# Performance work log

Measured on AMD Instinct MI355X. Metric: run time of the kernel, lower is better.

The kernel has to match this reference:

```python
import jax, jax.numpy as jnp
import numpy as np

H, D_MODEL, DK, DV = 16, 1024, 64, 64
B, S = 4, 2048
LN_EPS = 1e-6
NEG = -1e9


def setup_inputs() -> dict:
    key = jax.random.key(0)
    ks = jax.random.split(key, 8)
    query = jax.random.normal(ks[0], (B, S, D_MODEL), dtype=jnp.float32)
    k_in = jax.random.normal(ks[1], (B, S, D_MODEL), dtype=jnp.float32)
    v_in = jax.random.normal(ks[2], (B, S, D_MODEL), dtype=jnp.float32)
    mask = jax.random.randint(ks[3], (B, S, S), 0, 2, dtype=jnp.int32)
    sc = 1.0 / np.sqrt(D_MODEL)
    w_qs = jax.random.normal(ks[4], (D_MODEL, H * DK), dtype=jnp.float32) * sc
    w_ks = jax.random.normal(ks[5], (D_MODEL, H * DK), dtype=jnp.float32) * sc
    w_vs = jax.random.normal(ks[6], (D_MODEL, H * DV), dtype=jnp.float32) * sc
    w_out = jax.random.normal(ks[7], (H * DV, D_MODEL), dtype=jnp.float32) * (1.0 / np.sqrt(H * DV))
    ln_g = jnp.ones((D_MODEL,), dtype=jnp.float32)
    ln_b = jnp.zeros((D_MODEL,), dtype=jnp.float32)
    return {"query": query, "key": k_in, "value": v_in, "mask": mask,
            "w_qs": w_qs, "w_ks": w_ks, "w_vs": w_vs, "w_out": w_out,
            "ln_g": ln_g, "ln_b": ln_b}


def reference(query, key, value, mask, w_qs, w_ks, w_vs, w_out, ln_g, ln_b):
    # projections -> [B, H, S, dk/dv]
    q = (query @ w_qs).reshape(B, S, H, DK).transpose(0, 2, 1, 3)
    k = (key @ w_ks).reshape(B, S, H, DK).transpose(0, 2, 1, 3)
    v = (value @ w_vs).reshape(B, S, H, DV).transpose(0, 2, 1, 3)
    scores = jnp.einsum('bhqd,bhkd->bhqk', q, k) / np.sqrt(DK)
    scores = jnp.where(mask[:, None, :, :] == 0, NEG, scores)
    p = jax.nn.softmax(scores, axis=-1)  # dropout = identity in eval
    x = jnp.einsum('bhqk,bhkd->bhqd', p, v)  # [B,H,S,DV]
    x = x.transpose(0, 2, 1, 3).reshape(B, S, H * DV)
    out = x @ w_out + query  # dropout identity, residual
    mu = out.mean(-1, keepdims=True)
    var = out.var(-1, keepdims=True)
    return (out - mu) / jnp.sqrt(var + LN_EPS) * ln_g + ln_b
```

## Files before the change

kernel.cpp:

```cpp
#include <hip/hip_runtime.h>

#define BB   4
#define SS   2048
#define HH   16
#define DM   1024
#define DKV  64
#define LNEPS 1e-6f

#define MD_BF16 0
#define MD_F32  1
#define MD_F16  2

typedef __attribute__((ext_vector_type(8))) short bf16x8;
typedef __attribute__((ext_vector_type(4))) float f32x4;
#define MFMA16(a,b,c) __builtin_amdgcn_mfma_f32_16x16x32_bf16(a,b,c,0,0,0)

__device__ __forceinline__ void gl_lds16(const ushort* g, ushort* l) {
    __builtin_amdgcn_global_load_lds(
        (const __attribute__((address_space(1))) void*)g,
        (__attribute__((address_space(3))) void*)l, 16, 0, 0);
}
__device__ __forceinline__ void wait_vm0_barrier() {
    asm volatile("s_waitcnt vmcnt(0)" ::: "memory");
    __builtin_amdgcn_s_barrier();
}

__device__ __forceinline__ float2 unpack2(unsigned int u) {
    union { unsigned int i; float f; } a, b;
    a.i = u << 16;
    b.i = u & 0xffff0000u;
    return make_float2(a.f, b.f);
}
__device__ __forceinline__ unsigned short f2bf(float f) {
    union { float f; unsigned int i; } c; c.f = f;
    unsigned int u = c.i;
    unsigned int r = u + 0x7fffu + ((u >> 16) & 1u);
    return (unsigned short)(r >> 16);
}
__device__ __forceinline__ unsigned short f2bf_t(float f) {
    union { float f; unsigned int i; } c; c.f = f;
    return (unsigned short)(c.i >> 16);
}
__device__ __forceinline__ float h2f(unsigned int bits16) {
    unsigned short s = (unsigned short)bits16;
    _Float16 x;
    __builtin_memcpy(&x, &s, 2);
    return (float)x;
}
__device__ __forceinline__ void load4m(const void* p, int mode, size_t e0, float* o) {
    if (mode == MD_F32) {
        float4 v = *(const float4*)((const float*)p + e0);
        o[0] = v.x; o[1] = v.y; o[2] = v.z; o[3] = v.w;
    } else {
        uint2 u = *(const uint2*)((const ushort*)p + e0);
        if (mode == MD_BF16) {
            float2 a = unpack2(u.x), b = unpack2(u.y);
            o[0] = a.x; o[1] = a.y; o[2] = b.x; o[3] = b.y;
        } else {
            o[0] = h2f(u.x & 0xFFFFu); o[1] = h2f(u.x >> 16);
            o[2] = h2f(u.y & 0xFFFFu); o[3] = h2f(u.y >> 16);
        }
    }
}
__device__ __forceinline__ float loadS(const void* p, int mode, size_t i) {
    if (mode == MD_F32) return ((const float*)p)[i];
    unsigned short u = ((const ushort*)p)[i];
    if (mode == MD_BF16) { union { unsigned i; float f; } c; c.i = (unsigned)u << 16; return c.f; }
    return h2f(u);
}

__device__ __forceinline__ void loadAraw(const void* p, int m, size_t e, uint4* r) {
    if (m == MD_F32) {
        const float* f = (const float*)p + e;
        r[0] = *(const uint4*)(f);
        r[1] = *(const uint4*)(f + 4);
        r[2] = *(const uint4*)(f + 8);
        r[3] = *(const uint4*)(f + 12);
    } else {
        const ushort* s = (const ushort*)p + e;
        r[0] = *(const uint4*)s;
        r[1] = *(const uint4*)(s + 8);
    }
}
__device__ __forceinline__ void cvtA16(const uint4* r, int m, uint4* o2) {
    union { ushort u[16]; uint4 v[2]; } o;
    if (m == MD_F32) {
        const float* f = (const float*)r;
#pragma unroll
        for (int j = 0; j < 16; ++j) o.u[j] = f2bf(f[j]);
    } else if (m == MD_BF16) {
        o.v[0] = r[0]; o.v[1] = r[1];
    } else {
        const ushort* s = (const ushort*)r;
#pragma unroll
        for (int j = 0; j < 16; ++j) o.u[j] = f2bf(h2f(s[j]));
    }
    o2[0] = o.v[0]; o2[1] = o.v[1];
}

struct SniffArgs { const void* p[10]; int nhalf[10]; };

__global__ void sniff_all(SniffArgs a, int* __restrict__ modes) {
    __shared__ int cE, cO;
    const int slots[9] = {0, 1, 2, 4, 5, 6, 7, 8, 9};
    const int slot = slots[blockIdx.x];
    const ushort* p = (const ushort*)a.p[slot];
    const int nhalf = a.nhalf[slot];
    if (threadIdx.x == 0) { cE = 0; cO = 0; }
    __syncthreads();
    int e = 0, o = 0;
    for (int i = threadIdx.x; i < nhalf; i += 256) {
        unsigned ex = (p[i] >> 7) & 0xFFu;
        int hit = (ex < 100u || ex == 0xFFu) ? 1 : 0;
        if (i & 1) o += hit; else e += hit;
    }
    atomicAdd(&cE, e);
    atomicAdd(&cO, o);
    __syncthreads();
    if (threadIdx.x == 0) {
        int total = cE + cO;
        modes[slot] = (total < 48) ? MD_BF16 : ((cO * 4 < cE) ? MD_F32 : MD_F16);
    }
}

__global__ __launch_bounds__(256) void mpack(
    const int* __restrict__ mask, unsigned int* __restrict__ pm)
{
    const int w = blockIdx.x * 256 + threadIdx.x;
    const int* p = mask + (size_t)w * 32;
    unsigned int bits = 0u;
#pragma unroll
    for (int j = 0; j < 8; ++j) {
        int4 v = *(const int4*)(p + j * 4);
        bits |= (v.x ? 1u : 0u) << (4 * j);
        bits |= (v.y ? 1u : 0u) << (4 * j + 1);
        bits |= (v.z ? 1u : 0u) << (4 * j + 2);
        bits |= (v.w ? 1u : 0u) << (4 * j + 3);
    }
    pm[w] = bits;
}

struct WtArgs { const void* W[3]; ushort* Wt[3]; int slot[3]; };

__device__ __forceinline__ void wtrans_body(
    const void* __restrict__ W, ushort* __restrict__ Wt, int m)
{
    __shared__ ushort T[64][68];
    const int tid = threadIdx.x;
    const int k0 = blockIdx.y * 64, n0 = blockIdx.x * 64;

    const int r = tid >> 2, c = (tid & 3) * 16;
    float t[4];
#pragma unroll
    for (int j = 0; j < 4; ++j) {
        load4m(W, m, (size_t)(k0 + r) * DM + n0 + c + 4 * j, t);
#pragma unroll
        for (int i = 0; i < 4; ++i) T[r][c + 4 * j + i] = f2bf(t[i]);
    }
    __syncthreads();

    const int rn = tid >> 2, ck = (tid & 3) * 16;
    union { ushort u[8]; uint4 v; } p0, p1;
#pragma unroll
    for (int j = 0; j < 8; ++j) { p0.u[j] = T[ck + j][rn]; p1.u[j] = T[ck + 8 + j][rn]; }
    ushort* op = &Wt[(size_t)(n0 + rn) * DM + k0 + ck];
    *(uint4*)op = p0.v;
    *(uint4*)(op + 8) = p1.v;
}

__global__ __launch_bounds__(256) void wtrans3(WtArgs a, const int* __restrict__ modes) {
    const int g = blockIdx.z;
    wtrans_body(a.W[g], a.Wt[g], modes[a.slot[g]]);
}
__global__ __launch_bounds__(256) void wtrans(
    const void* __restrict__ W, ushort* __restrict__ Wt,
    const int* __restrict__ modes, int wslot)
{
    wtrans_body(W, Wt, modes[wslot]);
}

__global__ __launch_bounds__(256, 4) void projqkv(
    const void* __restrict__ Aq, const void* __restrict__ Ak, const void* __restrict__ Av,
    const ushort* __restrict__ Wtq, const ushort* __restrict__ Wtk, const ushort* __restrict__ Wtv,
    ushort* __restrict__ Qo, ushort* __restrict__ Ko, ushort* __restrict__ Vo,
    const int* __restrict__ modes)
{
    __shared__ __align__(16) ushort As[2][128 * 40];
    __shared__ __align__(16) ushort Bs[2][128 * 32];

    const int z = blockIdx.z;
    const void* A = (z == 0) ? Aq : (z == 1) ? Ak : Av;
    const ushort* Wt = (z == 0) ? Wtq : (z == 1) ? Wtk : Wtv;
    ushort* Out = (z == 0) ? Qo : (z == 1) ? Ko : Vo;
    const int vmode = (z == 2);
    const float scale = (z == 0) ? 0.125f : 1.0f;
    const int m = modes[z];

    const int tid = threadIdx.x;
    const int lane = tid & 63, wv = tid >> 6;
    const int quad = lane >> 4, L = lane & 15;
    const int bid = blockIdx.y * gridDim.x + blockIdx.x;
    const int swz = (bid & 7) * 64 + (bid >> 3);
    const int m0 = (swz >> 3) * 128, n0 = (swz & 7) * 128;
    const int wm = (wv >> 1) * 64, wn = (wv & 1) * 64;

    const int e0 = (wv * 2 + 0) * 512 + lane * 8;
    const int e1 = (wv * 2 + 1) * 512 + lane * 8;
    const ushort* gB0 = Wt + (size_t)(n0 + (e0 >> 5)) * DM + (e0 & 31);
    const ushort* gB1 = Wt + (size_t)(n0 + (e1 >> 5)) * DM + (e1 & 31);

    const int arow = tid >> 1, aseg = tid & 1;
    const size_t aoff = (size_t)(m0 + arow) * DM + aseg * 16;
    const int alds = arow * 40 + aseg * 16;

    f32x4 acc[4][4];
#pragma unroll
    for (int i = 0; i < 4; ++i)
#pragma unroll
        for (int j = 0; j < 4; ++j) { acc[i][j][0] = 0.f; acc[i][j][1] = 0.f; acc[i][j][2] = 0.f; acc[i][j][3] = 0.f; }

    {
        gl_lds16(gB0, &Bs[0][e0]);
        gl_lds16(gB1, &Bs[0][e1]);
        uint4 ar[4], ao[2];
        loadAraw(A, m, aoff, ar);
        cvtA16(ar, m, ao);
        *(uint4*)&As[0][alds]     = ao[0];
        *(uint4*)&As[0][alds + 8] = ao[1];
    }
    __syncthreads();

    int cur = 0;
    for (int kt = 0; kt < 31; ++kt) {
        const int kn = (kt + 1) * 32;
        const int nxt = cur ^ 1;
        gl_lds16(gB0 + kn, &Bs[nxt][e0]);
        gl_lds16(gB1 + kn, &Bs[nxt][e1]);
        uint4 ar[4], ao[2];
        loadAraw(A, m, aoff + kn, ar);

        bf16x8 af[4], bfr[4];
#pragma unroll
        for (int tm = 0; tm < 4; ++tm) af[tm] = *(const bf16x8*)&As[cur][(wm + tm * 16 + L) * 40 + quad * 8];
#pragma unroll
        for (int tn = 0; tn < 4; ++tn) bfr[tn] = *(const bf16x8*)&Bs[cur][(wn + tn * 16 + L) * 32 + quad * 8];
#pragma unroll
        for (int tm = 0; tm < 4; ++tm)
#pragma unroll
            for (int tn = 0; tn < 4; ++tn)
                acc[tm][tn] = MFMA16(af[tm], bfr[tn], acc[tm][tn]);

        cvtA16(ar, m, ao);
        *(uint4*)&As[nxt][alds]     = ao[0];
        *(uint4*)&As[nxt][alds + 8] = ao[1];

        __syncthreads();
        cur ^= 1;
    }
    {
        bf16x8 af[4], bfr[4];
#pragma unroll
        for (int tm = 0; tm < 4; ++tm) af[tm] = *(const bf16x8*)&As[cur][(wm + tm * 16 + L) * 40 + quad * 8];
#pragma unroll
        for (int tn = 0; tn < 4; ++tn) bfr[tn] = *(const bf16x8*)&Bs[cur][(wn + tn * 16 + L) * 32 + quad * 8];
#pragma unroll
        for (int tm = 0; tm < 4; ++tm)
#pragma unroll
            for (int tn = 0; tn < 4; ++tn)
                acc[tm][tn] = MFMA16(af[tm], bfr[tn], acc[tm][tn]);
    }

#pragma unroll
    for (int tm = 0; tm < 4; ++tm)
#pragma unroll
        for (int tn = 0; tn < 4; ++tn)
#pragma unroll
            for (int r = 0; r < 4; ++r) {
                const int mm = m0 + wm + tm * 16 + quad * 4 + r;
                const int n = n0 + wn + tn * 16 + L;
                const int b = mm >> 11, s = mm & 2047;
                const int h = n >> 6, d = n & 63;
                const size_t o = vmode
                    ? ((size_t)(b * HH + h) * DKV + d) * SS + s
                    : ((size_t)(b * HH + h) * SS + s) * DKV + d;
                Out[o] = f2bf(acc[tm][tn][r] * scale);
            }
}

__global__ __launch_bounds__(256) void attn_mfma(
    const ushort* __restrict__ Q, const ushort* __restrict__ K,
    const ushort* __restrict__ Vt, const unsigned int* __restrict__ pm,
    ushort* __restrict__ Xo)
{
    __shared__ __align__(16) ushort Ks[64][72];
    __shared__ __align__(16) ushort Vs[64][72];
    __shared__ __align__(16) ushort Ps[64][72];

    const int tid = threadIdx.x;
    const int lane = tid & 63, wv = tid >> 6;
    const int quad = lane >> 4, L = lane & 15;
    const int bid = blockIdx.y * gridDim.x + blockIdx.x;
    const int swz = (bid & 7) * 256 + (bid >> 3);
    const int bh = swz >> 5, b = bh >> 4, h = bh & 15;
    const int q0 = (swz & 31) * 64;

    const ushort* qp = &Q[((size_t)bh * SS + q0 + wv * 16 + L) * DKV + quad * 8];
    const bf16x8 aq0 = *(const bf16x8*)qp;
    const bf16x8 aq1 = *(const bf16x8*)(qp + 32);

    f32x4 O[4];
    float lacc[4];
#pragma unroll
    for (int t = 0; t < 4; ++t) { O[t][0] = 0.f; O[t][1] = 0.f; O[t][2] = 0.f; O[t][3] = 0.f; }
#pragma unroll
    for (int r = 0; r < 4; ++r) lacc[r] = 0.f;

    const int sr = tid >> 2, sg = tid & 3;
    const ushort* kbase = &K[((size_t)bh * SS + sr) * DKV + sg * 16];
    const ushort* vbase = &Vt[((size_t)bh * DKV + sr) * SS + sg * 16];
    const unsigned int* pmr[4];
#pragma unroll
    for (int r = 0; r < 4; ++r)
        pmr[r] = pm + ((size_t)b * SS + q0 + wv * 16 + quad * 4 + r) * 64;

    for (int kt = 0; kt < 32; ++kt) {
        __syncthreads();
        *(uint4*)&Ks[sr][sg * 16]     = *(const uint4*)kbase;
        *(uint4*)&Ks[sr][sg * 16 + 8] = *(const uint4*)(kbase + 8);
        *(uint4*)&Vs[sr][sg * 16]     = *(const uint4*)vbase;
        *(uint4*)&Vs[sr][sg * 16 + 8] = *(const uint4*)(vbase + 8);
        kbase += 64 * DKV;
        vbase += 64;

        uint2 mw[4];
#pragma unroll
        for (int r = 0; r < 4; ++r) mw[r] = *(const uint2*)(pmr[r] + 2 * kt);

        __syncthreads();

        f32x4 sc[4];
        __builtin_amdgcn_s_setprio(1);
#pragma unroll
        for (int t = 0; t < 4; ++t) {
            bf16x8 b0 = *(const bf16x8*)&Ks[t * 16 + L][quad * 8];
            bf16x8 b1 = *(const bf16x8*)&Ks[t * 16 + L][32 + quad * 8];
            f32x4 c; c[0] = 0.f; c[1] = 0.f; c[2] = 0.f; c[3] = 0.f;
            c = MFMA16(aq0, b0, c);
            c = MFMA16(aq1, b1, c);
            sc[t] = c;
        }
        __builtin_amdgcn_s_setprio(0);

#pragma unroll
        for (int r = 0; r < 4; ++r) {
            const unsigned mx = mw[r].x, my = mw[r].y;
#pragma unroll
            for (int t = 0; t < 4; ++t) {
                const float s = fminf(sc[t][r], 30.f);
                const float e = __expf(s);
                const unsigned wsel = (t & 2) ? my : mx;
                const float p = ((wsel >> ((t & 1) * 16 + L)) & 1u) ? e : 0.f;
                lacc[r] += p;
                Ps[wv * 16 + quad * 4 + r][t * 16 + L] = f2bf_t(p);
            }
        }

        bf16x8 ap0 = *(const bf16x8*)&Ps[wv * 16 + L][quad * 8];
        bf16x8 ap1 = *(const bf16x8*)&Ps[wv * 16 + L][32 + quad * 8];
        __builtin_amdgcn_s_setprio(1);
#pragma unroll
        for (int t = 0; t < 4; ++t) {
            bf16x8 v0 = *(const bf16x8*)&Vs[t * 16 + L][quad * 8];
            bf16x8 v1 = *(const bf16x8*)&Vs[t * 16 + L][32 + quad * 8];
            O[t] = MFMA16(ap0, v0, O[t]);
            O[t] = MFMA16(ap1, v1, O[t]);
        }
        __builtin_amdgcn_s_setprio(0);
    }

    float inv[4];
#pragma unroll
    for (int r = 0; r < 4; ++r) {
        float l = lacc[r];
#pragma unroll
        for (int off = 1; off < 16; off <<= 1) l += __shfl_xor(l, off, 64);
        inv[r] = 1.f / l;
    }
#pragma unroll
    for (int t = 0; t < 4; ++t)
#pragma unroll
        for (int r = 0; r < 4; ++r) {
            const int qg = q0 + wv * 16 + quad * 4 + r;
            Xo[((size_t)b * SS + qg) * DM + h * DKV + t * 16 + L] = f2bf(O[t][r] * inv[r]);
        }
}

__global__ __launch_bounds__(256) void oproj_mfma(
    const ushort* __restrict__ Xin, const ushort* __restrict__ Wt,
    const void* __restrict__ Qres, float* __restrict__ Out,
    const int* __restrict__ modes)
{
    __shared__ __align__(16) ushort Asf[2][4096];
    __shared__ __align__(16) ushort Bsf[2][4096];

    const int tid = threadIdx.x;
    const int lane = tid & 63, wv = tid >> 6;
    const int quad = lane >> 4, L = lane & 15;
    const int bid = blockIdx.y * gridDim.x + blockIdx.x;
    const int swz = (bid & 7) * 64 + (bid >> 3);
    const int m0 = (swz >> 3) * 128, n0 = (swz & 7) * 128;
    const int wm = (wv >> 1) * 64, wn = (wv & 1) * 64;
    const int mq = modes[0];

    const int e0 = (wv * 2 + 0) * 512 + lane * 8;
    const int e1 = (wv * 2 + 1) * 512 + lane * 8;
    const ushort* gA0 = Xin + (size_t)(m0 + (e0 >> 5)) * DM + (e0 & 31);
    const ushort* gA1 = Xin + (size_t)(m0 + (e1 >> 5)) * DM + (e1 & 31);
    const ushort* gB0 = Wt  + (size_t)(n0 + (e0 >> 5)) * DM + (e0 & 31);
    const ushort* gB1 = Wt  + (size_t)(n0 + (e1 >> 5)) * DM + (e1 & 31);

    f32x4 acc[4][4];
#pragma unroll
    for (int i = 0; i < 4; ++i)
#pragma unroll
        for (int j = 0; j < 4; ++j) { acc[i][j][0] = 0.f; acc[i][j][1] = 0.f; acc[i][j][2] = 0.f; acc[i][j][3] = 0.f; }

    gl_lds16(gA0, &Asf[0][e0]);
    gl_lds16(gA1, &Asf[0][e1]);
    gl_lds16(gB0, &Bsf[0][e0]);
    gl_lds16(gB1, &Bsf[0][e1]);
    wait_vm0_barrier();

    int cur = 0;
    for (int kt = 0; kt < 31; ++kt) {
        const int kn = (kt + 1) * 32;
        gl_lds16(gA0 + kn, &Asf[cur ^ 1][e0]);
        gl_lds16(gA1 + kn, &Asf[cur ^ 1][e1]);
        gl_lds16(gB0 + kn, &Bsf[cur ^ 1][e0]);
        gl_lds16(gB1 + kn, &Bsf[cur ^ 1][e1]);

        bf16x8 af[4], bfr[4];
#pragma unroll
        for (int tm = 0; tm < 4; ++tm) af[tm] = *(const bf16x8*)&Asf[cur][(wm + tm * 16 + L) * 32 + quad * 8];
#pragma unroll
        for (int tn = 0; tn < 4; ++tn) bfr[tn] = *(const bf16x8*)&Bsf[cur][(wn + tn * 16 + L) * 32 + quad * 8];
#pragma unroll
        for (int tm = 0; tm < 4; ++tm)
#pragma unroll
            for (int tn = 0; tn < 4; ++tn)
                acc[tm][tn] = MFMA16(af[tm], bfr[tn], acc[tm][tn]);

        wait_vm0_barrier();
        cur ^= 1;
    }
    {
        bf16x8 af[4], bfr[4];
#pragma unroll
        for (int tm = 0; tm < 4; ++tm) af[tm] = *(const bf16x8*)&Asf[cur][(wm + tm * 16 + L) * 32 + quad * 8];
#pragma unroll
        for (int tn = 0; tn < 4; ++tn) bfr[tn] = *(const bf16x8*)&Bsf[cur][(wn + tn * 16 + L) * 32 + quad * 8];
#pragma unroll
        for (int tm = 0; tm < 4; ++tm)
#pragma unroll
            for (int tn = 0; tn < 4; ++tn)
                acc[tm][tn] = MFMA16(af[tm], bfr[tn], acc[tm][tn]);
    }

#pragma unroll
    for (int tm = 0; tm < 4; ++tm)
#pragma unroll
        for (int tn = 0; tn < 4; ++tn)
#pragma unroll
            for (int r = 0; r < 4; ++r) {
                const int mm = m0 + wm + tm * 16 + quad * 4 + r;
                const int n = n0 + wn + tn * 16 + L;
                const size_t idx = (size_t)mm * DM + n;
                Out[idx] = acc[tm][tn][r] + loadS(Qres, mq, idx);
            }
}

__global__ __launch_bounds__(256) void ln_k(
    float* __restrict__ Out, const void* __restrict__ G,
    const void* __restrict__ Bt, const int* __restrict__ modes)
{
    const int tid = threadIdx.x, wv = tid >> 6, lane = tid & 63;
    const int row = blockIdx.x * 4 + wv;
    const int mg = modes[8], mb = modes[9];
    const size_t base = (size_t)row * DM + lane * 16;

    float v[16];
    float s = 0.f, q = 0.f;
#pragma unroll
    for (int j = 0; j < 16; j += 4) {
        float4 t = *(const float4*)&Out[base + j];
        v[j] = t.x; v[j+1] = t.y; v[j+2] = t.z; v[j+3] = t.w;
        s += t.x + t.y + t.z + t.w;
        q += t.x*t.x + t.y*t.y + t.z*t.z + t.w*t.w;
    }
#pragma unroll
    for (int off = 1; off < 64; off <<= 1) {
        s += __shfl_xor(s, off, 64);
        q += __shfl_xor(q, off, 64);
    }
    const float mu = s * (1.f / 1024.f);
    const float var = q * (1.f / 1024.f) - mu * mu;
    const float inv = rsqrtf(var + LNEPS);

    float gj[16], bj[16];
#pragma unroll
    for (int j = 0; j < 16; j += 4) {
        load4m(G,  mg, (size_t)lane * 16 + j, gj + j);
        load4m(Bt, mb, (size_t)lane * 16 + j, bj + j);
    }
#pragma unroll
    for (int j = 0; j < 16; j += 4) {
        float4 o;
        o.x = (v[j]   - mu) * inv * gj[j]   + bj[j];
        o.y = (v[j+1] - mu) * inv * gj[j+1] + bj[j+1];
        o.z = (v[j+2] - mu) * inv * gj[j+2] + bj[j+2];
        o.w = (v[j+3] - mu) * inv * gj[j+3] + bj[j+3];
        *(float4*)&Out[base + j] = o;
    }
}

extern "C" void kernel_launch(void* const* d_in, const int* in_sizes, int n_in,
                              void* d_out, int out_size, void* d_ws, size_t ws_size,
                              hipStream_t stream)
{
    const void* query = d_in[0];
    const void* key_i = d_in[1];
    const void* value = d_in[2];
    const int*  mask  = (const int*)d_in[3];
    const void* w_qs  = d_in[4];
    const void* w_ks  = d_in[5];
    const void* w_vs  = d_in[6];
    const void* w_out = d_in[7];
    const void* ln_g  = d_in[8];
    const void* ln_b  = d_in[9];
    float* out = (float*)d_out;

    int* modes = (int*)d_ws;
    const size_t PE = (size_t)BB * HH * SS * DKV;
    ushort* Qw = (ushort*)((char*)d_ws + 256);
    ushort* Kw = Qw + PE;
    ushort* Vw = Kw + PE;
    ushort* Xw = Vw + PE;
    ushort* Wtq  = (ushort*)((char*)d_out + (4  << 20));
    ushort* Wtk  = (ushort*)((char*)d_out + (8  << 20));
    ushort* Wtv  = (ushort*)((char*)d_out + (12 << 20));
    ushort* Wt2  = Qw;
    unsigned int* pmask = (unsigned int*)d_out;

    SniffArgs sa;
    for (int i = 0; i < 10; ++i) {
        sa.p[i] = d_in[i];
        sa.nhalf[i] = in_sizes[i] < 4096 ? in_sizes[i] : 4096;
    }
    sniff_all<<<9, 256, 0, stream>>>(sa, modes);
    mpack<<<2048, 256, 0, stream>>>(mask, pmask);

    WtArgs wa;
    wa.W[0] = w_qs; wa.Wt[0] = Wtq; wa.slot[0] = 4;
    wa.W[1] = w_ks; wa.Wt[1] = Wtk; wa.slot[1] = 5;
    wa.W[2] = w_vs; wa.Wt[2] = Wtv; wa.slot[2] = 6;
    wtrans3<<<dim3(16, 16, 3), 256, 0, stream>>>(wa, modes);

    projqkv<<<dim3(8, 64, 3), 256, 0, stream>>>(
        query, key_i, value, Wtq, Wtk, Wtv, Qw, Kw, Vw, modes);

    attn_mfma<<<dim3(32, 64), 256, 0, stream>>>(Qw, Kw, Vw, pmask, Xw);

    wtrans<<<dim3(16, 16), 256, 0, stream>>>(w_out, Wt2, modes, 7);
    oproj_mfma<<<dim3(8, 64), 256, 0, stream>>>(Xw, Wt2, query, out, modes);
    ln_k<<<2048, 256, 0, stream>>>(out, ln_g, ln_b, modes);
}
```

Baseline: 541.9 us.

## Merge prep kernels, inline dtype sniffing, register-prefetch GEMM pipelines

Folds the mask packing and all four weight transposes into one prep launch and drops the separate sniff kernel. Each kernel now detects input dtypes itself through a per-block sniff, which adds redundant global reads and barriers to every block. The projection and output GEMMs stop using global_load_lds and instead prefetch two k-steps ahead into registers, then store into padded LDS tiles with an explicit lgkmcnt wait and barrier. The output projection writes to a workspace buffer that LayerNorm then reads, so the Wt2 transpose can live in d_out.

```diff
diff --git a/kernel.cpp b/kernel.cpp
--- a/kernel.cpp
+++ b/kernel.cpp
@@ -14,16 +14,6 @@
 typedef __attribute__((ext_vector_type(8))) short bf16x8;
 typedef __attribute__((ext_vector_type(4))) float f32x4;
 #define MFMA16(a,b,c) __builtin_amdgcn_mfma_f32_16x16x32_bf16(a,b,c,0,0,0)
-
-__device__ __forceinline__ void gl_lds16(const ushort* g, ushort* l) {
-    __builtin_amdgcn_global_load_lds(
-        (const __attribute__((address_space(1))) void*)g,
-        (__attribute__((address_space(3))) void*)l, 16, 0, 0);
-}
-__device__ __forceinline__ void wait_vm0_barrier() {
-    asm volatile("s_waitcnt vmcnt(0)" ::: "memory");
-    __builtin_amdgcn_s_barrier();
-}
 
 __device__ __forceinline__ float2 unpack2(unsigned int u) {
     union { unsigned int i; float f; } a, b;
@@ -98,14 +88,9 @@
     o2[0] = o.v[0]; o2[1] = o.v[1];
 }
 
-struct SniffArgs { const void* p[10]; int nhalf[10]; };
-
-__global__ void sniff_all(SniffArgs a, int* __restrict__ modes) {
+__device__ __forceinline__ int sniff_local(const void* p_, int nhalf) {
     __shared__ int cE, cO;
-    const int slots[9] = {0, 1, 2, 4, 5, 6, 7, 8, 9};
-    const int slot = slots[blockIdx.x];
-    const ushort* p = (const ushort*)a.p[slot];
-    const int nhalf = a.nhalf[slot];
+    const ushort* p = (const ushort*)p_;
     if (threadIdx.x == 0) { cE = 0; cO = 0; }
     __syncthreads();
     int e = 0, o = 0;
@@ -117,37 +102,42 @@
     atomicAdd(&cE, e);
     atomicAdd(&cO, o);
     __syncthreads();
-    if (threadIdx.x == 0) {
-        int total = cE + cO;
-        modes[slot] = (total < 48) ? MD_BF16 : ((cO * 4 < cE) ? MD_F32 : MD_F16);
-    }
-}
-
-__global__ __launch_bounds__(256) void mpack(
-    const int* __restrict__ mask, unsigned int* __restrict__ pm)
+    const int total = cE + cO;
+    return (total < 48) ? MD_BF16 : ((cO * 4 < cE) ? MD_F32 : MD_F16);
+}
+
+__global__ __launch_bounds__(256) void prep(
+    const int* __restrict__ mask, unsigned int* __restrict__ pm,
+    const void* __restrict__ w_qs, const void* __restrict__ w_ks,
+    const void* __restrict__ w_vs, const void* __restrict__ w_out,
+    ushort* __restrict__ Wtq, ushort* __restrict__ Wtk,
+    ushort* __restrict__ Wtv, ushort* __restrict__ Wt2)
 {
-    const int w = blockIdx.x * 256 + threadIdx.x;
-    const int* p = mask + (size_t)w * 32;
-    unsigned int bits = 0u;
-#pragma unroll
-    for (int j = 0; j < 8; ++j) {
-        int4 v = *(const int4*)(p + j * 4);
-        bits |= (v.x ? 1u : 0u) << (4 * j);
-        bits |= (v.y ? 1u : 0u) << (4 * j + 1);
-        bits |= (v.z ? 1u : 0u) << (4 * j + 2);
-        bits |= (v.w ? 1u : 0u) << (4 * j + 3);
-    }
-    pm[w] = bits;
-}
-
-struct WtArgs { const void* W[3]; ushort* Wt[3]; int slot[3]; };
-
-__device__ __forceinline__ void wtrans_body(
-    const void* __restrict__ W, ushort* __restrict__ Wt, int m)
-{
+    const int bid = blockIdx.x;
+    if (bid < 2048) {
+        const int w = bid * 256 + threadIdx.x;
+        const int* p = mask + (size_t)w * 32;
+        unsigned int bits = 0u;
+#pragma unroll
+        for (int j = 0; j < 8; ++j) {
+            int4 v = *(const int4*)(p + j * 4);
+            bits |= (v.x ? 1u : 0u) << (4 * j);
+            bits |= (v.y ? 1u : 0u) << (4 * j + 1);
+            bits |= (v.z ? 1u : 0u) << (4 * j + 2);
+            bits |= (v.w ? 1u : 0u) << (4 * j + 3);
+        }
+        pm[w] = bits;
+        return;
+    }
+    const int b2 = bid - 2048;
+    const int g = b2 >> 8, sub = b2 & 255;
+    const void* W = (g == 0) ? w_qs : (g == 1) ? w_ks : (g == 2) ? w_vs : w_out;
+    ushort* Wt = (g == 0) ? Wtq : (g == 1) ? Wtk : (g == 2) ? Wtv : Wt2;
+    const int m = sniff_local(W, 4096);
+
     __shared__ ushort T[64][68];
     const int tid = threadIdx.x;
-    const int k0 = blockIdx.y * 64, n0 = blockIdx.x * 64;
+    const int n0 = (sub & 15) * 64, k0 = (sub >> 4) * 64;
 
     const int r = tid >> 2, c = (tid & 3) * 16;
     float t[4];
@@ -168,25 +158,13 @@
     *(uint4*)(op + 8) = p1.v;
 }
 
-__global__ __launch_bounds__(256) void wtrans3(WtArgs a, const int* __restrict__ modes) {
-    const int g = blockIdx.z;
-    wtrans_body(a.W[g], a.Wt[g], modes[a.slot[g]]);
-}
-__global__ __launch_bounds__(256) void wtrans(
-    const void* __restrict__ W, ushort* __restrict__ Wt,
-    const int* __restrict__ modes, int wslot)
-{
-    wtrans_body(W, Wt, modes[wslot]);
-}
-
-__global__ __launch_bounds__(256, 4) void projqkv(
+__global__ __launch_bounds__(256) void projqkv(
     const void* __restrict__ Aq, const void* __restrict__ Ak, const void* __restrict__ Av,
     const ushort* __restrict__ Wtq, const ushort* __restrict__ Wtk, const ushort* __restrict__ Wtv,
-    ushort* __restrict__ Qo, ushort* __restrict__ Ko, ushort* __restrict__ Vo,
-    const int* __restrict__ modes)
+    ushort* __restrict__ Qo, ushort* __restrict__ Ko, ushort* __restrict__ Vo)
 {
     __shared__ __align__(16) ushort As[2][128 * 40];
-    __shared__ __align__(16) ushort Bs[2][128 * 32];
+    __shared__ __align__(16) ushort Bs[2][128 * 40];
 
     const int z = blockIdx.z;
     const void* A = (z == 0) ? Aq : (z == 1) ? Ak : Av;
@@ -194,7 +172,7 @@
     ushort* Out = (z == 0) ? Qo : (z == 1) ? Ko : Vo;
     const int vmode = (z == 2);
     const float scale = (z == 0) ? 0.125f : 1.0f;
-    const int m = modes[z];
+    const int m = sniff_local(A, 4096);
 
     const int tid = threadIdx.x;
     const int lane = tid & 63, wv = tid >> 6;
@@ -204,14 +182,10 @@
     const int m0 = (swz >> 3) * 128, n0 = (swz & 7) * 128;
     const int wm = (wv >> 1) * 64, wn = (wv & 1) * 64;
 
-    const int e0 = (wv * 2 + 0) * 512 + lane * 8;
-    const int e1 = (wv * 2 + 1) * 512 + lane * 8;
-    const ushort* gB0 = Wt + (size_t)(n0 + (e0 >> 5)) * DM + (e0 & 31);
-    const ushort* gB1 = Wt + (size_t)(n0 + (e1 >> 5)) * DM + (e1 & 31);
-
     const int arow = tid >> 1, aseg = tid & 1;
     const size_t aoff = (size_t)(m0 + arow) * DM + aseg * 16;
-    const int alds = arow * 40 + aseg * 16;
+    const size_t boff = (size_t)(n0 + arow) * DM + aseg * 16;
+    const int slds = arow * 40 + aseg * 16;
 
     f32x4 acc[4][4];
 #pragma unroll
@@ -219,55 +193,56 @@
 #pragma unroll
         for (int j = 0; j < 4; ++j) { acc[i][j][0] = 0.f; acc[i][j][1] = 0.f; acc[i][j][2] = 0.f; acc[i][j][3] = 0.f; }
 
+    uint4 rA0[4], rA1[4], rB0[2], rB1[2];
+
+    loadAraw(A, m, aoff, rA0);
+    rB0[0] = *(const uint4*)(Wt + boff);
+    rB0[1] = *(const uint4*)(Wt + boff + 8);
     {
-        gl_lds16(gB0, &Bs[0][e0]);
-        gl_lds16(gB1, &Bs[0][e1]);
-        uint4 ar[4], ao[2];
-        loadAraw(A, m, aoff, ar);
-        cvtA16(ar, m, ao);
-        *(uint4*)&As[0][alds]     = ao[0];
-        *(uint4*)&As[0][alds + 8] = ao[1];
-    }
-    __syncthreads();
-
-    int cur = 0;
-    for (int kt = 0; kt < 31; ++kt) {
-        const int kn = (kt + 1) * 32;
-        const int nxt = cur ^ 1;
-        gl_lds16(gB0 + kn, &Bs[nxt][e0]);
-        gl_lds16(gB1 + kn, &Bs[nxt][e1]);
-        uint4 ar[4], ao[2];
-        loadAraw(A, m, aoff + kn, ar);
-
-        bf16x8 af[4], bfr[4];
-#pragma unroll
-        for (int tm = 0; tm < 4; ++tm) af[tm] = *(const bf16x8*)&As[cur][(wm + tm * 16 + L) * 40 + quad * 8];
-#pragma unroll
-        for (int tn = 0; tn < 4; ++tn) bfr[tn] = *(const bf16x8*)&Bs[cur][(wn + tn * 16 + L) * 32 + quad * 8];
-#pragma unroll
-        for (int tm = 0; tm < 4; ++tm)
-#pragma unroll
-            for (int tn = 0; tn < 4; ++tn)
-                acc[tm][tn] = MFMA16(af[tm], bfr[tn], acc[tm][tn]);
-
-        cvtA16(ar, m, ao);
-        *(uint4*)&As[nxt][alds]     = ao[0];
-        *(uint4*)&As[nxt][alds + 8] = ao[1];
-
-        __syncthreads();
-        cur ^= 1;
-    }
-    {
-        bf16x8 af[4], bfr[4];
-#pragma unroll
-        for (int tm = 0; tm < 4; ++tm) af[tm] = *(const bf16x8*)&As[cur][(wm + tm * 16 + L) * 40 + quad * 8];
-#pragma unroll
-        for (int tn = 0; tn < 4; ++tn) bfr[tn] = *(const bf16x8*)&Bs[cur][(wn + tn * 16 + L) * 32 + quad * 8];
-#pragma unroll
-        for (int tm = 0; tm < 4; ++tm)
-#pragma unroll
-            for (int tn = 0; tn < 4; ++tn)
-                acc[tm][tn] = MFMA16(af[tm], bfr[tn], acc[tm][tn]);
+        uint4 ao[2]; cvtA16(rA0, m, ao);
+        *(uint4*)&As[0][slds]     = ao[0];
+        *(uint4*)&As[0][slds + 8] = ao[1];
+        *(uint4*)&Bs[0][slds]     = rB0[0];
+        *(uint4*)&Bs[0][slds + 8] = rB0[1];
+    }
+    loadAraw(A, m, aoff + 32, rA1);
+    rB1[0] = *(const uint4*)(Wt + boff + 32);
+    rB1[1] = *(const uint4*)(Wt + boff + 40);
+    asm volatile("s_waitcnt lgkmcnt(0)" ::: "memory");
+    __builtin_amdgcn_s_barrier();
+    __builtin_amdgcn_sched_barrier(0);
+
+#define G_MFMA(P)                                                              \
+    { bf16x8 af[4], bfr[4];                                                    \
+      _Pragma("unroll") for (int tm = 0; tm < 4; ++tm)                         \
+          af[tm] = *(const bf16x8*)&As[P][(wm + tm * 16 + L) * 40 + quad * 8]; \
+      _Pragma("unroll") for (int tn = 0; tn < 4; ++tn)                         \
+          bfr[tn] = *(const bf16x8*)&Bs[P][(wn + tn * 16 + L) * 40 + quad * 8];\
+      _Pragma("unroll") for (int tm = 0; tm < 4; ++tm)                         \
+      _Pragma("unroll") for (int tn = 0; tn < 4; ++tn)                         \
+          acc[tm][tn] = MFMA16(af[tm], bfr[tn], acc[tm][tn]); }
+
+#define QKV_ITER(T, P, RAc, RBc, RAn, RBn)                                     \
+    { if ((T) + 2 < 32) {                                                      \
+          loadAraw(A, m, aoff + ((T) + 2) * 32, RAn);                          \
+          RBn[0] = *(const uint4*)(Wt + boff + ((T) + 2) * 32);                \
+          RBn[1] = *(const uint4*)(Wt + boff + ((T) + 2) * 32 + 8);            \
+      }                                                                        \
+      G_MFMA(P)                                                                \
+      if ((T) + 1 < 32) {                                                      \
+          uint4 ao[2]; cvtA16(RAc, m, ao);                                     \
+          *(uint4*)&As[(P) ^ 1][slds]     = ao[0];                             \
+          *(uint4*)&As[(P) ^ 1][slds + 8] = ao[1];                             \
+          *(uint4*)&Bs[(P) ^ 1][slds]     = RBc[0];                            \
+          *(uint4*)&Bs[(P) ^ 1][slds + 8] = RBc[1];                            \
+          asm volatile("s_waitcnt lgkmcnt(0)" ::: "memory");                   \
+          __builtin_amdgcn_s_barrier();                                        \
+          __builtin_amdgcn_sched_barrier(0);                                   \
+      } }
+
+    for (int tt = 0; tt < 16; ++tt) {
+        QKV_ITER(2 * tt,     0, rA1, rB1, rA0, rB0)
+        QKV_ITER(2 * tt + 1, 1, rA0, rB0, rA1, rB1)
     }
 
 #pragma unroll
@@ -397,11 +372,12 @@
 
 __global__ __launch_bounds__(256) void oproj_mfma(
     const ushort* __restrict__ Xin, const ushort* __restrict__ Wt,
-    const void* __restrict__ Qres, float* __restrict__ Out,
-    const int* __restrict__ modes)
+    const void* __restrict__ Qres, float* __restrict__ OutF)
 {
-    __shared__ __align__(16) ushort Asf[2][4096];
-    __shared__ __align__(16) ushort Bsf[2][4096];
+    __shared__ __align__(16) ushort As[2][128 * 40];
+    __shared__ __align__(16) ushort Bs[2][128 * 40];
+
+    const int mq = sniff_local(Qres, 4096);
 
     const int tid = threadIdx.x;
     const int lane = tid & 63, wv = tid >> 6;
@@ -410,14 +386,11 @@
     const int swz = (bid & 7) * 64 + (bid >> 3);
     const int m0 = (swz >> 3) * 128, n0 = (swz & 7) * 128;
     const int wm = (wv >> 1) * 64, wn = (wv & 1) * 64;
-    const int mq = modes[0];
-
-    const int e0 = (wv * 2 + 0) * 512 + lane * 8;
-    const int e1 = (wv * 2 + 1) * 512 + lane * 8;
-    const ushort* gA0 = Xin + (size_t)(m0 + (e0 >> 5)) * DM + (e0 & 31);
-    const ushort* gA1 = Xin + (size_t)(m0 + (e1 >> 5)) * DM + (e1 & 31);
-    const ushort* gB0 = Wt  + (size_t)(n0 + (e0 >> 5)) * DM + (e0 & 31);
-    const ushort* gB1 = Wt  + (size_t)(n0 + (e1 >> 5)) * DM + (e1 & 31);
+
+    const int arow = tid >> 1, aseg = tid & 1;
+    const size_t aoff = (size_t)(m0 + arow) * DM + aseg * 16;
+    const size_t boff = (size_t)(n0 + arow) * DM + aseg * 16;
+    const int slds = arow * 40 + aseg * 16;
 
     f32x4 acc[4][4];
 #pragma unroll
@@ -425,45 +398,45 @@
 #pragma unroll
         for (int j = 0; j < 4; ++j) { acc[i][j][0] = 0.f; acc[i][j][1] = 0.f; acc[i][j][2] = 0.f; acc[i][j][3] = 0.f; }
 
-    gl_lds16(gA0, &Asf[0][e0]);
-    gl_lds16(gA1, &Asf[0][e1]);
-    gl_lds16(gB0, &Bsf[0][e0]);
-    gl_lds16(gB1, &Bsf[0][e1]);
-    wait_vm0_barrier();
-
-    int cur = 0;
-    for (int kt = 0; kt < 31; ++kt) {
-        const int kn = (kt + 1) * 32;
-        gl_lds16(gA0 + kn, &Asf[cur ^ 1][e0]);
-        gl_lds16(gA1 + kn, &Asf[cur ^ 1][e1]);
-        gl_lds16(gB0 + kn, &Bsf[cur ^ 1][e0]);
-        gl_lds16(gB1 + kn, &Bsf[cur ^ 1][e1]);
-
-        bf16x8 af[4], bfr[4];
-#pragma unroll
-        for (int tm = 0; tm < 4; ++tm) af[tm] = *(const bf16x8*)&Asf[cur][(wm + tm * 16 + L) * 32 + quad * 8];
-#pragma unroll
-        for (int tn = 0; tn < 4; ++tn) bfr[tn] = *(const bf16x8*)&Bsf[cur][(wn + tn * 16 + L) * 32 + quad * 8];
-#pragma unroll
-        for (int tm = 0; tm < 4; ++tm)
-#pragma unroll
-            for (int tn = 0; tn < 4; ++tn)
-                acc[tm][tn] = MFMA16(af[tm], bfr[tn], acc[tm][tn]);
-
-        wait_vm0_barrier();
-        cur ^= 1;
-    }
-    {
-        bf16x8 af[4], bfr[4];
-#pragma unroll
-        for (int tm = 0; tm < 4; ++tm) af[tm] = *(const bf16x8*)&Asf[cur][(wm + tm * 16 + L) * 32 + quad * 8];
-#pragma unroll
-        for (int tn = 0; tn < 4; ++tn) bfr[tn] = *(const bf16x8*)&Bsf[cur][(wn + tn * 16 + L) * 32 + quad * 8];
-#pragma unroll
-        for (int tm = 0; tm < 4; ++tm)
-#pragma unroll
-            for (int tn = 0; tn < 4; ++tn)
-                acc[tm][tn] = MFMA16(af[tm], bfr[tn], acc[tm][tn]);
+    uint4 rA0[2], rA1[2], rB0[2], rB1[2];
+
+    rA0[0] = *(const uint4*)(Xin + aoff);
+    rA0[1] = *(const uint4*)(Xin + aoff + 8);
+    rB0[0] = *(const uint4*)(Wt + boff);
+    rB0[1] = *(const uint4*)(Wt + boff + 8);
+    *(uint4*)&As[0][slds]     = rA0[0];
+    *(uint4*)&As[0][slds + 8] = rA0[1];
+    *(uint4*)&Bs[0][slds]     = rB0[0];
+    *(uint4*)&Bs[0][slds + 8] = rB0[1];
+    rA1[0] = *(const uint4*)(Xin + aoff + 32);
+    rA1[1] = *(const uint4*)(Xin + aoff + 40);
+    rB1[0] = *(const uint4*)(Wt + boff + 32);
+    rB1[1] = *(const uint4*)(Wt + boff + 40);
+    asm volatile("s_waitcnt lgkmcnt(0)" ::: "memory");
+    __builtin_amdgcn_s_barrier();
+    __builtin_amdgcn_sched_barrier(0);
+
+#define OP_ITER(T, P, RAc, RBc, RAn, RBn)                                      \
+    { if ((T) + 2 < 32) {                                                      \
+          RAn[0] = *(const uint4*)(Xin + aoff + ((T) + 2) * 32);               \
+          RAn[1] = *(const uint4*)(Xin + aoff + ((T) + 2) * 32 + 8);           \
+          RBn[0] = *(const uint4*)(Wt + boff + ((T) + 2) * 32);                \
+          RBn[1] = *(const uint4*)(Wt + boff + ((T) + 2) * 32 + 8);            \
+      }                                                                        \
+      G_MFMA(P)                                                                \
+      if ((T) + 1 < 32) {                                                      \
+          *(uint4*)&As[(P) ^ 1][slds]     = RAc[0];                            \
+          *(uint4*)&As[(P) ^ 1][slds + 8] = RAc[1];                            \
+          *(uint4*)&Bs[(P) ^ 1][slds]     = RBc[0];                            \
+          *(uint4*)&Bs[(P) ^ 1][slds + 8] = RBc[1];                            \
+          asm volatile("s_waitcnt lgkmcnt(0)" ::: "memory");                   \
+          __builtin_amdgcn_s_barrier();                                        \
+          __builtin_amdgcn_sched_barrier(0);                                   \
+      } }
+
+    for (int tt = 0; tt < 16; ++tt) {
+        OP_ITER(2 * tt,     0, rA1, rB1, rA0, rB0)
+        OP_ITER(2 * tt + 1, 1, rA0, rB0, rA1, rB1)
     }
 
 #pragma unroll
@@ -475,24 +448,26 @@
                 const int mm = m0 + wm + tm * 16 + quad * 4 + r;
                 const int n = n0 + wn + tn * 16 + L;
                 const size_t idx = (size_t)mm * DM + n;
-                Out[idx] = acc[tm][tn][r] + loadS(Qres, mq, idx);
+                OutF[idx] = acc[tm][tn][r] + loadS(Qres, mq, idx);
             }
 }
 
 __global__ __launch_bounds__(256) void ln_k(
-    float* __restrict__ Out, const void* __restrict__ G,
-    const void* __restrict__ Bt, const int* __restrict__ modes)
+    const float* __restrict__ In, float* __restrict__ Out,
+    const void* __restrict__ G, const void* __restrict__ Bt)
 {
+    const int mg = sniff_local(G, 1024);
+    const int mb = sniff_local(Bt, 1024);
+
     const int tid = threadIdx.x, wv = tid >> 6, lane = tid & 63;
     const int row = blockIdx.x * 4 + wv;
-    const int mg = modes[8], mb = modes[9];
     const size_t base = (size_t)row * DM + lane * 16;
 
     float v[16];
     float s = 0.f, q = 0.f;
 #pragma unroll
     for (int j = 0; j < 16; j += 4) {
-        float4 t = *(const float4*)&Out[base + j];
+        float4 t = *(const float4*)&In[base + j];
         v[j] = t.x; v[j+1] = t.y; v[j+2] = t.z; v[j+3] = t.w;
         s += t.x + t.y + t.z + t.w;
         q += t.x*t.x + t.y*t.y + t.z*t.z + t.w*t.w;
@@ -539,38 +514,23 @@
     const void* ln_b  = d_in[9];
     float* out = (float*)d_out;
 
-    int* modes = (int*)d_ws;
     const size_t PE = (size_t)BB * HH * SS * DKV;
     ushort* Qw = (ushort*)((char*)d_ws + 256);
     ushort* Kw = Qw + PE;
     ushort* Vw = Kw + PE;
     ushort* Xw = Vw + PE;
-    ushort* Wtq  = (ushort*)((char*)d_out + (4  << 20));
-    ushort* Wtk  = (ushort*)((char*)d_out + (8  << 20));
-    ushort* Wtv  = (ushort*)((char*)d_out + (12 << 20));
-    ushort* Wt2  = Qw;
+    float*  OutF = (float*)Qw;
+    ushort* Wtq = (ushort*)((char*)d_out + (2 << 20));
+    ushort* Wtk = (ushort*)((char*)d_out + (4 << 20));
+    ushort* Wtv = (ushort*)((char*)d_out + (6 << 20));
+    ushort* Wt2 = (ushort*)((char*)d_out + (8 << 20));
     unsigned int* pmask = (unsigned int*)d_out;
 
-    SniffArgs sa;
-    for (int i = 0; i < 10; ++i) {
-        sa.p[i] = d_in[i];
-        sa.nhalf[i] = in_sizes[i] < 4096 ? in_sizes[i] : 4096;
-    }
-    sniff_all<<<9, 256, 0, stream>>>(sa, modes);
-    mpack<<<2048, 256, 0, stream>>>(mask, pmask);
-
-    WtArgs wa;
-    wa.W[0] = w_qs; wa.Wt[0] = Wtq; wa.slot[0] = 4;
-    wa.W[1] = w_ks; wa.Wt[1] = Wtk; wa.slot[1] = 5;
-    wa.W[2] = w_vs; wa.Wt[2] = Wtv; wa.slot[2] = 6;
-    wtrans3<<<dim3(16, 16, 3), 256, 0, stream>>>(wa, modes);
-
+    prep<<<3072, 256, 0, stream>>>(mask, pmask, w_qs, w_ks, w_vs, w_out,
+                                   Wtq, Wtk, Wtv, Wt2);
     projqkv<<<dim3(8, 64, 3), 256, 0, stream>>>(
-        query, key_i, value, Wtq, Wtk, Wtv, Qw, Kw, Vw, modes);
-
+        query, key_i, value, Wtq, Wtk, Wtv, Qw, Kw, Vw);
     attn_mfma<<<dim3(32, 64), 256, 0, stream>>>(Qw, Kw, Vw, pmask, Xw);
-
-    wtrans<<<dim3(16, 16), 256, 0, stream>>>(w_out, Wt2, modes, 7);
-    oproj_mfma<<<dim3(8, 64), 256, 0, stream>>>(Xw, Wt2, query, out, modes);
-    ln_k<<<2048, 256, 0, stream>>>(out, ln_g, ln_b, modes);
-}
+    oproj_mfma<<<dim3(8, 64), 256, 0, stream>>>(Xw, Wt2, query, OutF);
+    ln_k<<<2048, 256, 0, stream>>>(OutF, out, ln_g, ln_b);
+}
```

After: 661.6 us. 1.22x slower.
